# Performance work log

Measured on AMD Instinct MI355X. Metric: run time of the kernel, lower is better.

Reference implementation:

```python
import jax, jax.numpy as jnp
import numpy as np

B, S = 16, 8192
Q_DIM, K_DIM, ATTN_DIM = 512, 512, 512


def setup_inputs() -> dict:
    key = jax.random.key(0)
    k1, k2, k3, k4, k5, k6 = jax.random.split(key, 6)
    query = jax.random.normal(k1, (B, Q_DIM), dtype=jnp.float32)
    keys = jax.random.normal(k2, (B, S, K_DIM), dtype=jnp.float32)
    mask = jax.random.randint(k3, (B, S), 0, 2, dtype=jnp.int32)
    # learned params (torch Linear stores weight as [out, in]; we keep [in, out])
    Wq = jax.random.normal(k4, (Q_DIM, ATTN_DIM), dtype=jnp.float32) / np.sqrt(Q_DIM)
    Wk = jax.random.normal(k5, (K_DIM, ATTN_DIM), dtype=jnp.float32) / np.sqrt(K_DIM)
    v = jax.random.normal(k6, (ATTN_DIM,), dtype=jnp.float32) / np.sqrt(ATTN_DIM)
    return {"query": query, "keys": keys, "mask": mask, "Wq": Wq, "Wk": Wk, "v": v}


def reference(query, keys, mask, Wq, Wk, v):
    # q: [B, 1, A], k: [B, S, A]
    q = (query @ Wq)[:, None, :]
    k = jnp.einsum('bsk,ka->bsa', keys, Wk)
    # scores e: [B, S]  (v-projection reduces attn dim)
    e = jnp.einsum('bsa,a->bs', jnp.tanh(q + k), v)
    neg_min = jnp.finfo(e.dtype).min
    e = jnp.where(mask == 0, neg_min, e)
    a = jax.nn.softmax(e, axis=-1)  # [B, S]
    c = jnp.einsum('bs,bsk->bk', a, keys)  # context [B, K_DIM]
    return (c, a)
```

## Files before the change

kernel.cpp:

```cpp
#include <hip/hip_runtime.h>

#define BB 16
#define SS 8192
#define DD 512

typedef float  f32x4  __attribute__((ext_vector_type(4)));
typedef __bf16 bf16x8 __attribute__((ext_vector_type(8)));
typedef __bf16 bf16x4 __attribute__((ext_vector_type(4)));

__device__ __forceinline__ void cvt_store_bf4(unsigned short* dst, f32x4 v) {
    bf16x4 o;
    o.x = (__bf16)v.x; o.y = (__bf16)v.y; o.z = (__bf16)v.z; o.w = (__bf16)v.w;
    *(bf16x4*)dst = o;
}

__device__ __forceinline__ float tanh_fast(float x) {
    float e2 = __expf(2.0f * x);
    return 1.0f - 2.0f / (e2 + 1.0f);
}

__global__ __launch_bounds__(256) void prep_kernel(
    const float* __restrict__ query, const float* __restrict__ Wq,
    const float* __restrict__ Wk, float* __restrict__ qproj,
    unsigned short* __restrict__ WkT_f)
{
    __shared__ __bf16 lt[64][65];
    const int bid = blockIdx.x, t = threadIdx.x;
    if (bid < 64) {
        const int k0 = (bid >> 3) * 64, n0 = (bid & 7) * 64;
#pragma unroll
        for (int rep = 0; rep < 4; ++rep) {
            const int k = rep * 16 + (t >> 4), n = (t & 15) * 4;
            f32x4 vv = *(const f32x4*)&Wk[(size_t)(k0 + k) * DD + n0 + n];
            lt[k][n] = (__bf16)vv.x; lt[k][n + 1] = (__bf16)vv.y;
            lt[k][n + 2] = (__bf16)vv.z; lt[k][n + 3] = (__bf16)vv.w;
        }
        __syncthreads();
        const int g_loc = t >> 6, lane = t & 63;
        const int ml = lane & 15, quad = lane >> 4;
        const int g = (bid & 7) * 4 + g_loc;
#pragma unroll
        for (int j_loc = 0; j_loc < 2; ++j_loc) {
            const int j = (bid >> 3) * 2 + j_loc;
            bf16x8 o;
#pragma unroll
            for (int d = 0; d < 8; ++d)
                o[d] = lt[j_loc * 32 + quad * 8 + d][g_loc * 16 + ml];
            *(bf16x8*)&WkT_f[((size_t)((g * 16 + j) * 64 + lane)) * 8] = o;
        }
    } else {
        const int idx = (bid - 64) * 256 + t;
        const int b = idx >> 9;
        const int n = idx & 511;
        const float* q  = query + b * DD;
        const float* wp = Wq + n;
        float acc = 0.0f;
#pragma unroll 8
        for (int k = 0; k < DD; ++k)
            acc = fmaf(q[k], wp[(size_t)k * DD], acc);
        qproj[b * DD + n] = acc;
    }
}

__global__ __launch_bounds__(512, 4) void fused_kernel(
    const float* __restrict__ keys, const unsigned short* __restrict__ WkT_f,
    const float* __restrict__ qproj, const float* __restrict__ vvec,
    const int* __restrict__ mask, float* __restrict__ e_ws,
    float* __restrict__ cpart, float2* __restrict__ ml_ws)
{
    __shared__ unsigned short ksA[16 * 2048];
    __shared__ float sm_part[8][64];
    __shared__ float w_sh[64];
    __shared__ f32x4 red[3][128];

    const int tid  = threadIdx.x;
    const int w    = tid >> 6;
    const int lane = tid & 63;
    const int ml   = lane & 15;
    const int quad = lane >> 4;
    const int bid  = blockIdx.x;
    const int b    = bid >> 7;
    const int chunk = bid & 127;
    const int s0   = chunk << 6;

    const int m  = tid >> 3;
    const int q8 = tid & 7;
    const float* krow = keys + ((size_t)(b * SS + s0 + m)) * DD + q8 * 4;
    const int it = m >> 4;
    const int sq = q8 >> 1;
    const int j0 = (q8 & 1) * 4;
    const int base = it * 512 + ((m & 15) + 16 * sq) * 8 + j0;
    {
        f32x4 kst[8];
#pragma unroll
        for (int h = 0; h < 2; ++h) {
#pragma unroll
            for (int j = 0; j < 8; ++j)
                kst[j] = *(const f32x4*)(krow + (h * 8 + j) * 32);
#pragma unroll
            for (int j = 0; j < 8; ++j)
                cvt_store_bf4(&ksA[(h * 8 + j) * 2048 + base], kst[j]);
        }
    }
    __syncthreads();

    const unsigned short* wfb = WkT_f + (size_t)w * 32768 + lane * 8;

    f32x4 acc[4][4];
#pragma unroll
    for (int i = 0; i < 4; ++i)
#pragma unroll
        for (int jn = 0; jn < 4; ++jn) acc[i][jn] = (f32x4){0.f, 0.f, 0.f, 0.f};

#pragma unroll 4
    for (int j = 0; j < 16; ++j) {
        bf16x8 af[4];
#pragma unroll
        for (int i = 0; i < 4; ++i)
            af[i] = *(const bf16x8*)&ksA[j * 2048 + (i * 64 + lane) * 8];
#pragma unroll
        for (int jn = 0; jn < 4; ++jn) {
            bf16x8 bfr = *(const bf16x8*)(wfb + ((jn * 16 + j) << 9));
#pragma unroll
            for (int i = 0; i < 4; ++i)
                acc[i][jn] = __builtin_amdgcn_mfma_f32_16x16x32_bf16(af[i], bfr, acc[i][jn], 0, 0, 0);
        }
    }

    float qv[4], vv[4];
#pragma unroll
    for (int jn = 0; jn < 4; ++jn) {
        const int n = w * 64 + jn * 16 + ml;
        qv[jn] = qproj[b * DD + n];
        vv[jn] = vvec[n];
    }
#pragma unroll
    for (int i = 0; i < 4; ++i) {
#pragma unroll
        for (int r = 0; r < 4; ++r) {
            float s = 0.0f;
#pragma unroll
            for (int jn = 0; jn < 4; ++jn) {
                float xx = acc[i][jn][r] + qv[jn];
                s += tanh_fast(xx) * vv[jn];
            }
            s += __shfl_xor(s, 1, 64);
            s += __shfl_xor(s, 2, 64);
            s += __shfl_xor(s, 4, 64);
            s += __shfl_xor(s, 8, 64);
            if (ml == 0) sm_part[w][i * 16 + quad * 4 + r] = s;
        }
    }
    __syncthreads();

    if (tid < 64) {
        float e = sm_part[0][tid] + sm_part[1][tid] + sm_part[2][tid] + sm_part[3][tid]
                + sm_part[4][tid] + sm_part[5][tid] + sm_part[6][tid] + sm_part[7][tid];
        const int mk = mask[b * SS + s0 + tid];
        if (mk == 0) e = -3.402823466e38f;
        e_ws[(size_t)b * SS + s0 + tid] = e;
        float mx = e;
#pragma unroll
        for (int off = 32; off >= 1; off >>= 1) mx = fmaxf(mx, __shfl_xor(mx, off, 64));
        float wv = (mk == 0) ? 0.0f : __expf(e - mx);
        float l  = wv;
#pragma unroll
        for (int off = 32; off >= 1; off >>= 1) l += __shfl_xor(l, off, 64);
        w_sh[tid] = wv;
        if (tid == 0) ml_ws[b * 128 + chunk] = make_float2(mx, l);
    }
    __syncthreads();

    const int n4 = (tid & 127) << 2;
    const int sh = tid >> 7;
    const float* kctx = keys + ((size_t)(b * SS + s0 + sh * 16)) * DD + n4;
    f32x4 cacc = (f32x4){0.f, 0.f, 0.f, 0.f};
#pragma unroll 8
    for (int sI = 0; sI < 16; ++sI) {
        float wgt = w_sh[sh * 16 + sI];
        f32x4 kv  = *(const f32x4*)(kctx + (size_t)sI * DD);
        cacc += kv * wgt;
    }
    if (sh) red[sh - 1][tid & 127] = cacc;
    __syncthreads();
    if (sh == 0) {
        cacc += red[0][tid] + red[1][tid] + red[2][tid];
        *(f32x4*)(cpart + ((size_t)(b * 128 + chunk)) * 512 + n4) = cacc;
    }
}

__global__ __launch_bounds__(256) void finalize_kernel(
    const float* __restrict__ e_ws, const float* __restrict__ cpart,
    const float2* __restrict__ ml_ws, float* __restrict__ out)
{
    __shared__ float rm[4], rs[4];
    __shared__ float sc_sh[128];
    __shared__ float cred[4][512];
    const int bid = blockIdx.x, t = threadIdx.x;
    const int b = (bid < 16) ? bid : ((bid - 16) >> 3);

    float mi = -3.402823466e38f, li = 0.0f;
    if (t < 128) { float2 p = ml_ws[b * 128 + t]; mi = p.x; li = p.y; }
    float mr = mi;
#pragma unroll
    for (int off = 32; off >= 1; off >>= 1) mr = fmaxf(mr, __shfl_xor(mr, off, 64));
    if ((t & 63) == 0) rm[t >> 6] = mr;
    __syncthreads();
    const float M = fmaxf(fmaxf(rm[0], rm[1]), fmaxf(rm[2], rm[3]));
    float si = (t < 128) ? li * __expf(mi - M) : 0.0f;
#pragma unroll
    for (int off = 32; off >= 1; off >>= 1) si += __shfl_xor(si, off, 64);
    if ((t & 63) == 0) rs[t >> 6] = si;
    __syncthreads();
    const float L = rs[0] + rs[1] + rs[2] + rs[3];
    const float invL = 1.0f / L;

    if (bid < 16) {
        if (t < 128) sc_sh[t] = __expf(ml_ws[b * 128 + t].x - M);
        __syncthreads();
        const int w2 = t >> 6, l = t & 63;
        float pa[8] = {0.f, 0.f, 0.f, 0.f, 0.f, 0.f, 0.f, 0.f};
#pragma unroll 4
        for (int i = w2 * 32; i < w2 * 32 + 32; ++i) {
            const float sc = sc_sh[i];
            const float* cp = cpart + ((size_t)(b * 128 + i)) * 512 + l * 8;
#pragma unroll
            for (int c = 0; c < 8; ++c) pa[c] = fmaf(cp[c], sc, pa[c]);
        }
#pragma unroll
        for (int c = 0; c < 8; ++c) cred[w2][l * 8 + c] = pa[c];
        __syncthreads();
#pragma unroll
        for (int rep = 0; rep < 2; ++rep) {
            const int n = t + rep * 256;
            out[b * DD + n] = (cred[0][n] + cred[1][n] + cred[2][n] + cred[3][n]) * invL;
        }
    } else {
        const int chunk8 = (bid - 16) & 7;
        const float* ep = e_ws + (size_t)b * SS + chunk8 * 1024;
        float* ap = out + BB * DD + (size_t)b * SS + chunk8 * 1024;
#pragma unroll
        for (int r = 0; r < 4; ++r) {
            float e = ep[t + 256 * r];
            ap[t + 256 * r] = __expf(e - M) * invL;
        }
    }
}

extern "C" void kernel_launch(void* const* d_in, const int* in_sizes, int n_in,
                              void* d_out, int out_size, void* d_ws, size_t ws_size,
                              hipStream_t stream)
{
    const float* query = (const float*)d_in[0];
    const float* keys  = (const float*)d_in[1];
    const int*   mask  = (const int*)  d_in[2];
    const float* Wq    = (const float*)d_in[3];
    const float* Wk    = (const float*)d_in[4];
    const float* v     = (const float*)d_in[5];
    float* out = (float*)d_out;

    float*          qproj = (float*)d_ws;
    unsigned short* WkT_f = (unsigned short*)((char*)d_ws + 32768);
    float*          e_ws  = (float*)((char*)d_ws + 32768 + 524288);
    float*          cpart = (float*)((char*)d_ws + 32768 + 2 * 524288);
    float2*         ml_ws = (float2*)((char*)d_ws + 32768 + 2 * 524288 + 4194304);

    prep_kernel    <<<96, 256, 0, stream>>>(query, Wq, Wk, qproj, WkT_f);
    fused_kernel   <<<BB * (SS / 64), 512, 0, stream>>>(keys, WkT_f, qproj, v, mask,
                                                        e_ws, cpart, ml_ws);
    finalize_kernel<<<16 + 128, 256, 0, stream>>>(e_ws, cpart, ml_ws, out);
}
```

Measured before the change: 490.3 us.

## Make fused kernel persistent over four chunks with double-buffered key staging

Each block now handles four consecutive 64-row chunks instead of one (512 blocks instead of 2048). The K dimension is split into two halves, each with its own LDS buffer, so global loads and bf16 conversion of the next half or chunk overlap with the MFMA work on the current one. This is meant to hide global load latency and cut block launch and prologue overhead. The cost is fewer blocks in flight, more register pressure from the staging registers alongside the accumulators, and extra barriers.

```diff
diff --git a/kernel.cpp b/kernel.cpp
--- a/kernel.cpp
+++ b/kernel.cpp
@@ -62,13 +62,51 @@
     }
 }
 
+__device__ __forceinline__ void k_half(
+    f32x4 (&acc)[4][4], const unsigned short* __restrict__ ksrc,
+    const unsigned short* __restrict__ wfbh,
+    const float* __restrict__ stage_src, unsigned short* __restrict__ stage_dst,
+    const int sbase, const bool do_stage, const int lane)
+{
+#pragma unroll
+    for (int q = 0; q < 2; ++q) {
+        f32x4 kst[4];
+        if (do_stage) {
+#pragma unroll
+            for (int j = 0; j < 4; ++j)
+                kst[j] = *(const f32x4*)(stage_src + (q * 4 + j) * 32);
+        }
+#pragma unroll
+        for (int jj = 0; jj < 4; ++jj) {
+            const int j = q * 4 + jj;
+            bf16x8 af[4];
+#pragma unroll
+            for (int i = 0; i < 4; ++i)
+                af[i] = *(const bf16x8*)&ksrc[j * 2048 + (i * 64 + lane) * 8];
+#pragma unroll
+            for (int jn = 0; jn < 4; ++jn) {
+                bf16x8 bfr = *(const bf16x8*)(wfbh + ((jn * 16 + j) << 9));
+#pragma unroll
+                for (int i = 0; i < 4; ++i)
+                    acc[i][jn] = __builtin_amdgcn_mfma_f32_16x16x32_bf16(af[i], bfr, acc[i][jn], 0, 0, 0);
+            }
+        }
+        if (do_stage) {
+#pragma unroll
+            for (int j = 0; j < 4; ++j)
+                cvt_store_bf4(&stage_dst[(q * 4 + j) * 2048 + sbase], kst[j]);
+        }
+    }
+    __syncthreads();
+}
+
 __global__ __launch_bounds__(512, 4) void fused_kernel(
     const float* __restrict__ keys, const unsigned short* __restrict__ WkT_f,
     const float* __restrict__ qproj, const float* __restrict__ vvec,
     const int* __restrict__ mask, float* __restrict__ e_ws,
     float* __restrict__ cpart, float2* __restrict__ ml_ws)
 {
-    __shared__ unsigned short ksA[16 * 2048];
+    __shared__ unsigned short ks[2][8 * 2048];
     __shared__ float sm_part[8][64];
     __shared__ float w_sh[64];
     __shared__ f32x4 red[3][128];
@@ -79,113 +117,105 @@
     const int ml   = lane & 15;
     const int quad = lane >> 4;
     const int bid  = blockIdx.x;
-    const int b    = bid >> 7;
-    const int chunk = bid & 127;
-    const int s0   = chunk << 6;
+    const int b    = bid >> 5;
+    const int c0   = (bid & 31) << 2;
 
     const int m  = tid >> 3;
     const int q8 = tid & 7;
-    const float* krow = keys + ((size_t)(b * SS + s0 + m)) * DD + q8 * 4;
     const int it = m >> 4;
     const int sq = q8 >> 1;
-    const int j0 = (q8 & 1) * 4;
-    const int base = it * 512 + ((m & 15) + 16 * sq) * 8 + j0;
+    const int j0q = (q8 & 1) * 4;
+    const int sbase = it * 512 + ((m & 15) + 16 * sq) * 8 + j0q;
+    const float* krow0 = keys + ((size_t)(b * SS + c0 * 64 + m)) * DD + q8 * 4;
+
+    const unsigned short* wfb = WkT_f + (size_t)w * 32768 + lane * 8;
+
     {
         f32x4 kst[8];
 #pragma unroll
-        for (int h = 0; h < 2; ++h) {
-#pragma unroll
-            for (int j = 0; j < 8; ++j)
-                kst[j] = *(const f32x4*)(krow + (h * 8 + j) * 32);
-#pragma unroll
-            for (int j = 0; j < 8; ++j)
-                cvt_store_bf4(&ksA[(h * 8 + j) * 2048 + base], kst[j]);
-        }
+        for (int j = 0; j < 8; ++j) kst[j] = *(const f32x4*)(krow0 + j * 32);
+#pragma unroll
+        for (int j = 0; j < 8; ++j) cvt_store_bf4(&ks[0][j * 2048 + sbase], kst[j]);
     }
     __syncthreads();
 
-    const unsigned short* wfb = WkT_f + (size_t)w * 32768 + lane * 8;
-
-    f32x4 acc[4][4];
-#pragma unroll
-    for (int i = 0; i < 4; ++i)
-#pragma unroll
-        for (int jn = 0; jn < 4; ++jn) acc[i][jn] = (f32x4){0.f, 0.f, 0.f, 0.f};
-
-#pragma unroll 4
-    for (int j = 0; j < 16; ++j) {
-        bf16x8 af[4];
+#pragma unroll 1
+    for (int t = 0; t < 4; ++t) {
+        const int c  = c0 + t;
+        const int s0 = c << 6;
+        const float* krow = krow0 + (size_t)t * 32768;
+
+        int mk = 0;
+        if (tid < 64) mk = mask[(size_t)b * SS + s0 + tid];
+
+        f32x4 acc[4][4];
 #pragma unroll
         for (int i = 0; i < 4; ++i)
-            af[i] = *(const bf16x8*)&ksA[j * 2048 + (i * 64 + lane) * 8];
+#pragma unroll
+            for (int jn = 0; jn < 4; ++jn) acc[i][jn] = (f32x4){0.f, 0.f, 0.f, 0.f};
+
+        k_half(acc, ks[0], wfb,        krow + 256,   ks[1], sbase, true,  lane);
+        k_half(acc, ks[1], wfb + 4096, krow + 32768, ks[0], sbase, t < 3, lane);
+
+        float qv[4], vv[4];
 #pragma unroll
         for (int jn = 0; jn < 4; ++jn) {
-            bf16x8 bfr = *(const bf16x8*)(wfb + ((jn * 16 + j) << 9));
-#pragma unroll
-            for (int i = 0; i < 4; ++i)
-                acc[i][jn] = __builtin_amdgcn_mfma_f32_16x16x32_bf16(af[i], bfr, acc[i][jn], 0, 0, 0);
-        }
-    }
-
-    float qv[4], vv[4];
-#pragma unroll
-    for (int jn = 0; jn < 4; ++jn) {
-        const int n = w * 64 + jn * 16 + ml;
-        qv[jn] = qproj[b * DD + n];
-        vv[jn] = vvec[n];
-    }
-#pragma unroll
-    for (int i = 0; i < 4; ++i) {
-#pragma unroll
-        for (int r = 0; r < 4; ++r) {
-            float s = 0.0f;
-#pragma unroll
-            for (int jn = 0; jn < 4; ++jn) {
-                float xx = acc[i][jn][r] + qv[jn];
-                s += tanh_fast(xx) * vv[jn];
+            const int n = w * 64 + jn * 16 + ml;
+            qv[jn] = qproj[b * DD + n];
+            vv[jn] = vvec[n];
+        }
+#pragma unroll
+        for (int i = 0; i < 4; ++i) {
+#pragma unroll
+            for (int r = 0; r < 4; ++r) {
+                float s = 0.0f;
+#pragma unroll
+                for (int jn = 0; jn < 4; ++jn) {
+                    float xx = acc[i][jn][r] + qv[jn];
+                    s += tanh_fast(xx) * vv[jn];
+                }
+                s += __shfl_xor(s, 1, 64);
+                s += __shfl_xor(s, 2, 64);
+                s += __shfl_xor(s, 4, 64);
+                s += __shfl_xor(s, 8, 64);
+                if (ml == 0) sm_part[w][i * 16 + quad * 4 + r] = s;
             }
-            s += __shfl_xor(s, 1, 64);
-            s += __shfl_xor(s, 2, 64);
-            s += __shfl_xor(s, 4, 64);
-            s += __shfl_xor(s, 8, 64);
-            if (ml == 0) sm_part[w][i * 16 + quad * 4 + r] = s;
-        }
-    }
-    __syncthreads();
-
-    if (tid < 64) {
-        float e = sm_part[0][tid] + sm_part[1][tid] + sm_part[2][tid] + sm_part[3][tid]
-                + sm_part[4][tid] + sm_part[5][tid] + sm_part[6][tid] + sm_part[7][tid];
-        const int mk = mask[b * SS + s0 + tid];
-        if (mk == 0) e = -3.402823466e38f;
-        e_ws[(size_t)b * SS + s0 + tid] = e;
-        float mx = e;
-#pragma unroll
-        for (int off = 32; off >= 1; off >>= 1) mx = fmaxf(mx, __shfl_xor(mx, off, 64));
-        float wv = (mk == 0) ? 0.0f : __expf(e - mx);
-        float l  = wv;
-#pragma unroll
-        for (int off = 32; off >= 1; off >>= 1) l += __shfl_xor(l, off, 64);
-        w_sh[tid] = wv;
-        if (tid == 0) ml_ws[b * 128 + chunk] = make_float2(mx, l);
-    }
-    __syncthreads();
-
-    const int n4 = (tid & 127) << 2;
-    const int sh = tid >> 7;
-    const float* kctx = keys + ((size_t)(b * SS + s0 + sh * 16)) * DD + n4;
-    f32x4 cacc = (f32x4){0.f, 0.f, 0.f, 0.f};
+        }
+        __syncthreads();
+
+        if (tid < 64) {
+            float e = sm_part[0][tid] + sm_part[1][tid] + sm_part[2][tid] + sm_part[3][tid]
+                    + sm_part[4][tid] + sm_part[5][tid] + sm_part[6][tid] + sm_part[7][tid];
+            if (mk == 0) e = -3.402823466e38f;
+            e_ws[(size_t)b * SS + s0 + tid] = e;
+            float mx = e;
+#pragma unroll
+            for (int off = 32; off >= 1; off >>= 1) mx = fmaxf(mx, __shfl_xor(mx, off, 64));
+            float wv = (mk == 0) ? 0.0f : __expf(e - mx);
+            float l  = wv;
+#pragma unroll
+            for (int off = 32; off >= 1; off >>= 1) l += __shfl_xor(l, off, 64);
+            w_sh[tid] = wv;
+            if (tid == 0) ml_ws[b * 128 + c] = make_float2(mx, l);
+        }
+        __syncthreads();
+
+        const int n4 = (tid & 127) << 2;
+        const int sh = tid >> 7;
+        const float* kctx = keys + ((size_t)(b * SS + s0 + sh * 16)) * DD + n4;
+        f32x4 cacc = (f32x4){0.f, 0.f, 0.f, 0.f};
 #pragma unroll 8
-    for (int sI = 0; sI < 16; ++sI) {
-        float wgt = w_sh[sh * 16 + sI];
-        f32x4 kv  = *(const f32x4*)(kctx + (size_t)sI * DD);
-        cacc += kv * wgt;
-    }
-    if (sh) red[sh - 1][tid & 127] = cacc;
-    __syncthreads();
-    if (sh == 0) {
-        cacc += red[0][tid] + red[1][tid] + red[2][tid];
-        *(f32x4*)(cpart + ((size_t)(b * 128 + chunk)) * 512 + n4) = cacc;
+        for (int sI = 0; sI < 16; ++sI) {
+            float wgt = w_sh[sh * 16 + sI];
+            f32x4 kv  = *(const f32x4*)(kctx + (size_t)sI * DD);
+            cacc += kv * wgt;
+        }
+        if (sh) red[sh - 1][tid & 127] = cacc;
+        __syncthreads();
+        if (sh == 0) {
+            cacc += red[0][tid] + red[1][tid] + red[2][tid];
+            *(f32x4*)(cpart + ((size_t)(b * 128 + c)) * 512 + n4) = cacc;
+        }
     }
 }
 
@@ -266,7 +296,7 @@
     float2*         ml_ws = (float2*)((char*)d_ws + 32768 + 2 * 524288 + 4194304);
 
     prep_kernel    <<<96, 256, 0, stream>>>(query, Wq, Wk, qproj, WkT_f);
-    fused_kernel   <<<BB * (SS / 64), 512, 0, stream>>>(keys, WkT_f, qproj, v, mask,
-                                                        e_ws, cpart, ml_ws);
+    fused_kernel   <<<512, 512, 0, stream>>>(keys, WkT_f, qproj, v, mask,
+                                             e_ws, cpart, ml_ws);
     finalize_kernel<<<16 + 128, 256, 0, stream>>>(e_ws, cpart, ml_ws, out);
 }
```

After: 739.9 us. 1.51x slower.

## Reuse bf16 keys in LDS for context sum instead of re-reading global

Applied to the files above, without the earlier changes.

The context accumulation now reads the bf16 copy of the key tile already staged in shared memory, replacing a second fp32 read of keys from global memory. A rotated index spreads the LDS accesses across banks. Key loads become nontemporal, and the mask load is hoisted to the start of the kernel. The change halves global key traffic for a memory-bound kernel, but the context is now computed from bf16-rounded keys, which lowers its precision.

```diff
diff --git a/kernel.cpp b/kernel.cpp
--- a/kernel.cpp
+++ b/kernel.cpp
@@ -83,6 +83,9 @@
     const int chunk = bid & 127;
     const int s0   = chunk << 6;
 
+    int mk = 0;
+    if (tid < 64) mk = mask[(size_t)b * SS + s0 + tid];
+
     const int m  = tid >> 3;
     const int q8 = tid & 7;
     const float* krow = keys + ((size_t)(b * SS + s0 + m)) * DD + q8 * 4;
@@ -96,7 +99,8 @@
         for (int h = 0; h < 2; ++h) {
 #pragma unroll
             for (int j = 0; j < 8; ++j)
-                kst[j] = *(const f32x4*)(krow + (h * 8 + j) * 32);
+                kst[j] = __builtin_nontemporal_load(
+                             (const f32x4*)(krow + (h * 8 + j) * 32));
 #pragma unroll
             for (int j = 0; j < 8; ++j)
                 cvt_store_bf4(&ksA[(h * 8 + j) * 2048 + base], kst[j]);
@@ -156,7 +160,6 @@
     if (tid < 64) {
         float e = sm_part[0][tid] + sm_part[1][tid] + sm_part[2][tid] + sm_part[3][tid]
                 + sm_part[4][tid] + sm_part[5][tid] + sm_part[6][tid] + sm_part[7][tid];
-        const int mk = mask[b * SS + s0 + tid];
         if (mk == 0) e = -3.402823466e38f;
         e_ws[(size_t)b * SS + s0 + tid] = e;
         float mx = e;
@@ -171,20 +174,29 @@
     }
     __syncthreads();
 
-    const int n4 = (tid & 127) << 2;
-    const int sh = tid >> 7;
-    const float* kctx = keys + ((size_t)(b * SS + s0 + sh * 16)) * DD + n4;
+    const int l   = tid & 127;
+    const int sh  = tid >> 7;
+    const int n4  = l << 2;
+    const int jq  = l >> 3;
+    const int qd  = (l >> 1) & 3;
+    const int d0  = (l & 1) * 4;
+    const int cbase = jq * 2048 + sh * 512 + qd * 128 + d0;
+    const int rot   = (l & 15) + (l >> 3);
     f32x4 cacc = (f32x4){0.f, 0.f, 0.f, 0.f};
-#pragma unroll 8
-    for (int sI = 0; sI < 16; ++sI) {
-        float wgt = w_sh[sh * 16 + sI];
-        f32x4 kv  = *(const f32x4*)(kctx + (size_t)sI * DD);
-        cacc += kv * wgt;
-    }
-    if (sh) red[sh - 1][tid & 127] = cacc;
+#pragma unroll
+    for (int p = 0; p < 16; ++p) {
+        const int sI = (p + rot) & 15;
+        bf16x4 kv = *(const bf16x4*)&ksA[cbase + sI * 8];
+        const float wgt = w_sh[sh * 16 + sI];
+        cacc.x += wgt * (float)kv.x;
+        cacc.y += wgt * (float)kv.y;
+        cacc.z += wgt * (float)kv.z;
+        cacc.w += wgt * (float)kv.w;
+    }
+    if (sh) red[sh - 1][l] = cacc;
     __syncthreads();
     if (sh == 0) {
-        cacc += red[0][tid] + red[1][tid] + red[2][tid];
+        cacc += red[0][l] + red[1][l] + red[2][l];
         *(f32x4*)(cpart + ((size_t)(b * 128 + chunk)) * 512 + n4) = cacc;
     }
 }
```

Result: faster. 458.5 us (-6.5%).
